# Performance work log

Hardware: AMD Instinct MI355X
Metric: run time of the kernel (lower is better)

## Reference

```python
import jax, jax.numpy as jnp
import numpy as np

N_HEADS = 16

def setup_inputs() -> dict:
    key = jax.random.key(0)
    k1, k2 = jax.random.split(key)
    qkv = jax.random.normal(k1, (4, 3072, 2048), dtype=jnp.float32)
    encoder_kv = jax.random.normal(k2, (4, 2048, 256), dtype=jnp.float32)
    return {"qkv": qkv, "encoder_kv": encoder_kv}

def reference(qkv, encoder_kv):
    bs, width, length = qkv.shape
    ch = width // (3 * N_HEADS)  # 64
    # [bs*H, 3*ch, T] -> q, k, v each [bs*H, ch, T]
    q, k, v = jnp.split(qkv.reshape(bs * N_HEADS, 3 * ch, length), 3, axis=1)
    # encoder kv: [bs, H*2*ch, S] -> ek, ev each [bs*H, ch, S]
    ek, ev = jnp.split(encoder_kv.reshape(bs * N_HEADS, 2 * ch, -1), 2, axis=1)
    k = jnp.concatenate([ek, k], axis=-1)  # [bs*H, ch, S+T]
    v = jnp.concatenate([ev, v], axis=-1)
    scale = ch ** -0.25  # 1/sqrt(sqrt(ch)), applied to both q and k
    weight = jnp.einsum('bct,bcs->bts', q * scale, k * scale)  # [bs*H, T, S+T]
    weight = jax.nn.softmax(weight.astype(jnp.float32), axis=-1).astype(qkv.dtype)
    a = jnp.einsum('bts,bcs->bct', weight, v)  # [bs*H, ch, T]
    return a.reshape(bs, -1, length)
```

## Files before the change

### kernel.cpp

```cpp
#include <hip/hip_runtime.h>
#include <hip/hip_bf16.h>

typedef __attribute__((ext_vector_type(8))) short bf16x8;
typedef __attribute__((ext_vector_type(4))) float f32x4;
typedef __attribute__((ext_vector_type(4))) unsigned u32x4;
typedef __attribute__((ext_vector_type(2))) unsigned u32x2;

#define T_LEN 2048
#define S_ENC 256
#define QSCALE 0.18033688011112042f

#define BARRIER()                                         \
  do {                                                    \
    asm volatile("s_waitcnt lgkmcnt(0)" ::: "memory");    \
    __builtin_amdgcn_s_barrier();                         \
  } while (0)

__device__ __forceinline__ float exp2_hw(float x) {
#if __has_builtin(__builtin_amdgcn_exp2f)
  return __builtin_amdgcn_exp2f(x);
#else
  float r;
  asm("v_exp_f32 %0, %1" : "=v"(r) : "v"(x));
  return r;
#endif
}

__device__ __forceinline__ unsigned cvt_pk_bf16(float lo, float hi) {
  unsigned r;
  asm("v_cvt_pk_bf16_f32 %0, %1, %2" : "=v"(r) : "v"(lo), "v"(hi));
  return r;
}

__device__ __forceinline__ short f2bf(float x) {
  union { __hip_bfloat16 b; short s; } u;
  u.b = __float2bfloat16(x);
  return u.s;
}

__device__ __forceinline__ int swz(int row, int col) {
  return row * 64 + (col ^ ((row & 7) << 3));
}

union PU { u32x4 u; bf16x8 b; };

template<int STRIDE>
__device__ __forceinline__ void tile_body(
    const float* __restrict__ kb, const float* __restrict__ vb, int s0,
    short* __restrict__ Kt, short* __restrict__ Vt,
    const bf16x8 (&qf)[4][2], f32x4 (&o)[4][4], float (&lp)[4], int tid) {

  const int lane = tid & 63;
  const int ln = lane & 15;
  const int lg = lane >> 4;

  const int ks = tid & 63;
  const int kc = (tid >> 6) * 8;
  float kr[8], kr2[8];
  const float* kp = kb + (size_t)kc * STRIDE + (s0 + ks);
  const float* kp2 = kp + (size_t)32 * STRIDE;
#pragma unroll
  for (int r = 0; r < 8; ++r) kr[r] = kp[(size_t)r * STRIDE];
#pragma unroll
  for (int r = 0; r < 8; ++r) kr2[r] = kp2[(size_t)r * STRIDE];

  const int vg = tid & 15;
  const int vc = tid >> 4;
  const float* vp0 = vb + (size_t)vc * STRIDE + (s0 + 4 * vg);
  f32x4 vr0 = *(const f32x4*)(vp0);
  f32x4 vr1 = *(const f32x4*)(vp0 + (size_t)32 * STRIDE);
  f32x4 vr2 = *(const f32x4*)(vp0 + (size_t)16 * STRIDE);
  f32x4 vr3 = *(const f32x4*)(vp0 + (size_t)48 * STRIDE);

  BARRIER();

  u32x4 kw;
#pragma unroll
  for (int r = 0; r < 4; ++r) kw[r] = cvt_pk_bf16(kr[2 * r], kr[2 * r + 1]);
  *(u32x4*)(Kt + swz(ks, kc)) = kw;
  u32x4 kw2;
#pragma unroll
  for (int r = 0; r < 4; ++r) kw2[r] = cvt_pk_bf16(kr2[2 * r], kr2[2 * r + 1]);
  *(u32x4*)(Kt + swz(ks, kc + 32)) = kw2;

  const int vcol = 32 * (vg >> 3) + 8 * (vg & 3) + 4 * ((vg >> 2) & 1);
  u32x2 vw;
  vw[0] = cvt_pk_bf16(vr0[0], vr0[1]);
  vw[1] = cvt_pk_bf16(vr0[2], vr0[3]);
  *(u32x2*)(Vt + swz(vc, vcol)) = vw;
  vw[0] = cvt_pk_bf16(vr1[0], vr1[1]);
  vw[1] = cvt_pk_bf16(vr1[2], vr1[3]);
  *(u32x2*)(Vt + swz(vc + 32, vcol)) = vw;
  vw[0] = cvt_pk_bf16(vr2[0], vr2[1]);
  vw[1] = cvt_pk_bf16(vr2[2], vr2[3]);
  *(u32x2*)(Vt + swz(vc + 16, vcol)) = vw;
  vw[0] = cvt_pk_bf16(vr3[0], vr3[1]);
  vw[1] = cvt_pk_bf16(vr3[2], vr3[3]);
  *(u32x2*)(Vt + swz(vc + 48, vcol)) = vw;

  BARRIER();

  bf16x8 kf[4][2];
#pragma unroll
  for (int mt = 0; mt < 4; ++mt) {
    const int row = 16 * mt + ln;
    kf[mt][0] = *(const bf16x8*)(Kt + swz(row, 8 * lg));
    kf[mt][1] = *(const bf16x8*)(Kt + swz(row, 32 + 8 * lg));
  }

  PU pfrag[4][2];
#pragma unroll
  for (int pr = 0; pr < 2; ++pr) {
    f32x4 sacc[2][4];
#pragma unroll
    for (int q2 = 0; q2 < 2; ++q2)
#pragma unroll
      for (int mt = 0; mt < 4; ++mt) sacc[q2][mt] = (f32x4){0.f, 0.f, 0.f, 0.f};

#pragma unroll
    for (int mt = 0; mt < 4; ++mt)
#pragma unroll
      for (int q2 = 0; q2 < 2; ++q2) {
        const int qt = 2 * pr + q2;
        sacc[q2][mt] = __builtin_amdgcn_mfma_f32_16x16x32_bf16(kf[mt][0], qf[qt][0], sacc[q2][mt], 0, 0, 0);
        sacc[q2][mt] = __builtin_amdgcn_mfma_f32_16x16x32_bf16(kf[mt][1], qf[qt][1], sacc[q2][mt], 0, 0, 0);
      }

#pragma unroll
    for (int q2 = 0; q2 < 2; ++q2) {
      const int qt = 2 * pr + q2;
      float pmt[4];
#pragma unroll
      for (int mt = 0; mt < 4; ++mt) {
        float p0 = exp2_hw(sacc[q2][mt][0]);
        float p1 = exp2_hw(sacc[q2][mt][1]);
        float p2 = exp2_hw(sacc[q2][mt][2]);
        float p3 = exp2_hw(sacc[q2][mt][3]);
        pfrag[qt][mt >> 1].u[2 * (mt & 1) + 0] = cvt_pk_bf16(p0, p1);
        pfrag[qt][mt >> 1].u[2 * (mt & 1) + 1] = cvt_pk_bf16(p2, p3);
        pmt[mt] = (p0 + p1) + (p2 + p3);
      }
      lp[qt] += (pmt[0] + pmt[1]) + (pmt[2] + pmt[3]);
    }
  }

#pragma unroll
  for (int sub = 0; sub < 2; ++sub)
#pragma unroll
    for (int ct = 0; ct < 4; ++ct) {
      const bf16x8 vf = *(const bf16x8*)(Vt + swz(16 * ct + ln, 32 * sub + 8 * lg));
#pragma unroll
      for (int qt = 0; qt < 4; ++qt)
        o[qt][ct] = __builtin_amdgcn_mfma_f32_16x16x32_bf16(vf, pfrag[qt][sub].b, o[qt][ct], 0, 0, 0);
    }
}

__global__ __launch_bounds__(256, 2) void attn_kernel(
    const float* __restrict__ qkv, const float* __restrict__ ekv,
    float* __restrict__ out) {
  const int tid = threadIdx.x;
  const int lane = tid & 63;
  const int wave = tid >> 6;
  const int ln = lane & 15;
  const int lg = lane >> 4;

  const int bh = blockIdx.x & 63;
  const int qb = blockIdx.x >> 6;
  const int t0 = qb * 256 + wave * 64;

  const float* qp  = qkv + (size_t)bh * 192 * T_LEN;
  const float* kp  = qp + (size_t)64 * T_LEN;
  const float* vp  = qp + (size_t)128 * T_LEN;
  const float* ekp = ekv + (size_t)bh * 128 * S_ENC;
  const float* evp = ekp + (size_t)64 * S_ENC;

  __shared__ __attribute__((aligned(16))) short Kt[64 * 64];
  __shared__ __attribute__((aligned(16))) short Vt[64 * 64];

  bf16x8 qf[4][2];
#pragma unroll
  for (int qt = 0; qt < 4; ++qt)
#pragma unroll
    for (int kk = 0; kk < 2; ++kk)
#pragma unroll
      for (int j = 0; j < 8; ++j)
        qf[qt][kk][j] =
            f2bf(qp[(size_t)(32 * kk + 8 * lg + j) * T_LEN + (t0 + 16 * qt + ln)] * QSCALE);

  f32x4 o[4][4];
#pragma unroll
  for (int qt = 0; qt < 4; ++qt)
#pragma unroll
    for (int ct = 0; ct < 4; ++ct) o[qt][ct] = (f32x4){0.f, 0.f, 0.f, 0.f};
  float lp[4] = {0.f, 0.f, 0.f, 0.f};

  for (int st = 0; st < 4; ++st)
    tile_body<S_ENC>(ekp, evp, 64 * st, Kt, Vt, qf, o, lp, tid);
  for (int st = 0; st < 32; ++st)
    tile_body<T_LEN>(kp, vp, 64 * st, Kt, Vt, qf, o, lp, tid);

#pragma unroll
  for (int qt = 0; qt < 4; ++qt) {
    float l = lp[qt];
    l += __shfl_xor(l, 16);
    l += __shfl_xor(l, 32);
    const float inv = 1.0f / l;
    float* ob = out + (size_t)bh * 64 * T_LEN + (t0 + 16 * qt + ln);
#pragma unroll
    for (int ct = 0; ct < 4; ++ct)
#pragma unroll
      for (int r = 0; r < 4; ++r)
        ob[(size_t)(16 * ct + 4 * lg + r) * T_LEN] = o[qt][ct][r] * inv;
  }
}

extern "C" void kernel_launch(void* const* d_in, const int* in_sizes, int n_in,
                              void* d_out, int out_size, void* d_ws, size_t ws_size,
                              hipStream_t stream) {
  const float* qkv = (const float*)d_in[0];
  const float* ekv = (const float*)d_in[1];
  float* out = (float*)d_out;
  attn_kernel<<<dim3(512), dim3(256), 0, stream>>>(qkv, ekv, out);
}
```

Baseline: 90.12 us.

## Double-buffer K/V shared tiles and prefetch next tile during compute

Splits the per-tile body into global load, LDS staging write and compute phases. The self-attention loop now keeps two LDS buffers, so the next tile is written while the current one is computed and the tile after that is prefetched into registers, with one barrier per iteration instead of two. This is meant to hide global load latency behind MFMA work. In exchange it doubles LDS use, raises register pressure from holding prefetched data across compute, and switches the custom barrier macro to __syncthreads.

```diff
diff --git a/kernel.cpp b/kernel.cpp
--- a/kernel.cpp
+++ b/kernel.cpp
@@ -10,11 +10,7 @@
 #define S_ENC 256
 #define QSCALE 0.18033688011112042f
 
-#define BARRIER()                                         \
-  do {                                                    \
-    asm volatile("s_waitcnt lgkmcnt(0)" ::: "memory");    \
-    __builtin_amdgcn_s_barrier();                         \
-  } while (0)
+#define BARRIER() __syncthreads()
 
 __device__ __forceinline__ float exp2_hw(float x) {
 #if __has_builtin(__builtin_amdgcn_exp2f)
@@ -45,60 +41,59 @@
 union PU { u32x4 u; bf16x8 b; };
 
 template<int STRIDE>
-__device__ __forceinline__ void tile_body(
-    const float* __restrict__ kb, const float* __restrict__ vb, int s0,
-    short* __restrict__ Kt, short* __restrict__ Vt,
+__device__ __forceinline__ void issue_loads(
+    const float* __restrict__ kb, const float* __restrict__ vb, int s0, int tid,
+    float (&kr)[8], float (&kr2)[8], f32x4 (&vr)[4]) {
+  const int ks = tid & 63;
+  const int kc = (tid >> 6) * 8;
+  const float* kp = kb + (size_t)kc * STRIDE + (s0 + ks);
+  const float* kp2 = kp + (size_t)32 * STRIDE;
+#pragma unroll
+  for (int r = 0; r < 8; ++r) kr[r] = kp[(size_t)r * STRIDE];
+#pragma unroll
+  for (int r = 0; r < 8; ++r) kr2[r] = kp2[(size_t)r * STRIDE];
+  const int vg = tid & 15;
+  const int vc = tid >> 4;
+  const float* vp0 = vb + (size_t)vc * STRIDE + (s0 + 4 * vg);
+  vr[0] = *(const f32x4*)(vp0);
+  vr[1] = *(const f32x4*)(vp0 + (size_t)32 * STRIDE);
+  vr[2] = *(const f32x4*)(vp0 + (size_t)16 * STRIDE);
+  vr[3] = *(const f32x4*)(vp0 + (size_t)48 * STRIDE);
+}
+
+__device__ __forceinline__ void stage_write(
+    short* __restrict__ Kt, short* __restrict__ Vt, int tid,
+    const float (&kr)[8], const float (&kr2)[8], const f32x4 (&vr)[4]) {
+  const int ks = tid & 63;
+  const int kc = (tid >> 6) * 8;
+  u32x4 kw;
+#pragma unroll
+  for (int r = 0; r < 4; ++r) kw[r] = cvt_pk_bf16(kr[2 * r], kr[2 * r + 1]);
+  *(u32x4*)(Kt + swz(ks, kc)) = kw;
+  u32x4 kw2;
+#pragma unroll
+  for (int r = 0; r < 4; ++r) kw2[r] = cvt_pk_bf16(kr2[2 * r], kr2[2 * r + 1]);
+  *(u32x4*)(Kt + swz(ks, kc + 32)) = kw2;
+
+  const int vg = tid & 15;
+  const int vc = tid >> 4;
+  const int vcol = 32 * (vg >> 3) + 8 * (vg & 3) + 4 * ((vg >> 2) & 1);
+  const int vrow[4] = {vc, vc + 32, vc + 16, vc + 48};
+#pragma unroll
+  for (int i = 0; i < 4; ++i) {
+    u32x2 vw;
+    vw[0] = cvt_pk_bf16(vr[i][0], vr[i][1]);
+    vw[1] = cvt_pk_bf16(vr[i][2], vr[i][3]);
+    *(u32x2*)(Vt + swz(vrow[i], vcol)) = vw;
+  }
+}
+
+__device__ __forceinline__ void compute_tile(
+    const short* __restrict__ Kt, const short* __restrict__ Vt,
     const bf16x8 (&qf)[4][2], f32x4 (&o)[4][4], float (&lp)[4], int tid) {
-
   const int lane = tid & 63;
   const int ln = lane & 15;
   const int lg = lane >> 4;
-
-  const int ks = tid & 63;
-  const int kc = (tid >> 6) * 8;
-  float kr[8], kr2[8];
-  const float* kp = kb + (size_t)kc * STRIDE + (s0 + ks);
-  const float* kp2 = kp + (size_t)32 * STRIDE;
-#pragma unroll
-  for (int r = 0; r < 8; ++r) kr[r] = kp[(size_t)r * STRIDE];
-#pragma unroll
-  for (int r = 0; r < 8; ++r) kr2[r] = kp2[(size_t)r * STRIDE];
-
-  const int vg = tid & 15;
-  const int vc = tid >> 4;
-  const float* vp0 = vb + (size_t)vc * STRIDE + (s0 + 4 * vg);
-  f32x4 vr0 = *(const f32x4*)(vp0);
-  f32x4 vr1 = *(const f32x4*)(vp0 + (size_t)32 * STRIDE);
-  f32x4 vr2 = *(const f32x4*)(vp0 + (size_t)16 * STRIDE);
-  f32x4 vr3 = *(const f32x4*)(vp0 + (size_t)48 * STRIDE);
-
-  BARRIER();
-
-  u32x4 kw;
-#pragma unroll
-  for (int r = 0; r < 4; ++r) kw[r] = cvt_pk_bf16(kr[2 * r], kr[2 * r + 1]);
-  *(u32x4*)(Kt + swz(ks, kc)) = kw;
-  u32x4 kw2;
-#pragma unroll
-  for (int r = 0; r < 4; ++r) kw2[r] = cvt_pk_bf16(kr2[2 * r], kr2[2 * r + 1]);
-  *(u32x4*)(Kt + swz(ks, kc + 32)) = kw2;
-
-  const int vcol = 32 * (vg >> 3) + 8 * (vg & 3) + 4 * ((vg >> 2) & 1);
-  u32x2 vw;
-  vw[0] = cvt_pk_bf16(vr0[0], vr0[1]);
-  vw[1] = cvt_pk_bf16(vr0[2], vr0[3]);
-  *(u32x2*)(Vt + swz(vc, vcol)) = vw;
-  vw[0] = cvt_pk_bf16(vr1[0], vr1[1]);
-  vw[1] = cvt_pk_bf16(vr1[2], vr1[3]);
-  *(u32x2*)(Vt + swz(vc + 32, vcol)) = vw;
-  vw[0] = cvt_pk_bf16(vr2[0], vr2[1]);
-  vw[1] = cvt_pk_bf16(vr2[2], vr2[3]);
-  *(u32x2*)(Vt + swz(vc + 16, vcol)) = vw;
-  vw[0] = cvt_pk_bf16(vr3[0], vr3[1]);
-  vw[1] = cvt_pk_bf16(vr3[2], vr3[3]);
-  *(u32x2*)(Vt + swz(vc + 48, vcol)) = vw;
-
-  BARRIER();
 
   bf16x8 kf[4][2];
 #pragma unroll
@@ -174,8 +169,8 @@
   const float* ekp = ekv + (size_t)bh * 128 * S_ENC;
   const float* evp = ekp + (size_t)64 * S_ENC;
 
-  __shared__ __attribute__((aligned(16))) short Kt[64 * 64];
-  __shared__ __attribute__((aligned(16))) short Vt[64 * 64];
+  __shared__ __attribute__((aligned(16))) short Kt[2][64 * 64];
+  __shared__ __attribute__((aligned(16))) short Vt[2][64 * 64];
 
   bf16x8 qf[4][2];
 #pragma unroll
@@ -194,10 +189,37 @@
     for (int ct = 0; ct < 4; ++ct) o[qt][ct] = (f32x4){0.f, 0.f, 0.f, 0.f};
   float lp[4] = {0.f, 0.f, 0.f, 0.f};
 
-  for (int st = 0; st < 4; ++st)
-    tile_body<S_ENC>(ekp, evp, 64 * st, Kt, Vt, qf, o, lp, tid);
-  for (int st = 0; st < 32; ++st)
-    tile_body<T_LEN>(kp, vp, 64 * st, Kt, Vt, qf, o, lp, tid);
+  for (int st = 0; st < 4; ++st) {
+    float kr[8], kr2[8];
+    f32x4 vr[4];
+    issue_loads<S_ENC>(ekp, evp, 64 * st, tid, kr, kr2, vr);
+    BARRIER();
+    stage_write(&Kt[0][0], &Vt[0][0], tid, kr, kr2, vr);
+    BARRIER();
+    compute_tile(&Kt[0][0], &Vt[0][0], qf, o, lp, tid);
+  }
+
+  {
+    float kr[8], kr2[8];
+    f32x4 vr[4];
+    issue_loads<T_LEN>(kp, vp, 0, tid, kr, kr2, vr);
+    BARRIER();
+    stage_write(&Kt[0][0], &Vt[0][0], tid, kr, kr2, vr);
+    issue_loads<T_LEN>(kp, vp, 64, tid, kr, kr2, vr);
+    BARRIER();
+
+    int cur = 0;
+#pragma unroll 1
+    for (int t = 0; t < 31; ++t) {
+      stage_write(&Kt[cur ^ 1][0], &Vt[cur ^ 1][0], tid, kr, kr2, vr);
+      if (t < 30)
+        issue_loads<T_LEN>(kp, vp, 64 * (t + 2), tid, kr, kr2, vr);
+      compute_tile(&Kt[cur][0], &Vt[cur][0], qf, o, lp, tid);
+      BARRIER();
+      cur ^= 1;
+    }
+    compute_tile(&Kt[cur][0], &Vt[cur][0], qf, o, lp, tid);
+  }
 
 #pragma unroll
   for (int qt = 0; qt < 4; ++qt) {
```

New measurement: 98.77 us. +9.6%, slower.
